# Optimization experiments

Hardware: AMD Instinct MI355X
Metric: run time of the kernel (lower is better)

The kernel has to match this reference:

```python
import jax, jax.numpy as jnp
import numpy as np

EPS = 1e-5
NUM_HEAD = 8
HEAD_DIM = 64
SCALE = HEAD_DIM ** -0.5


def setup_inputs() -> dict:
    key = jax.random.key(0)
    ks = jax.random.split(key, 3)
    b, n, dim = 4, 2048, 512
    inner = NUM_HEAD * HEAD_DIM  # 512
    x = jax.random.normal(ks[0], (b, n, dim), dtype=jnp.float32)
    ln_w = jnp.ones((dim,), jnp.float32)
    ln_b = jnp.zeros((dim,), jnp.float32)
    qkv_w = jax.random.normal(ks[1], (3 * inner, dim), jnp.float32) * (dim ** -0.5)
    qkv_b = jnp.zeros((3 * inner,), jnp.float32)
    out_w = jax.random.normal(ks[2], (dim, inner), jnp.float32) * (inner ** -0.5)
    out_b = jnp.zeros((dim,), jnp.float32)
    return {"x": x, "ln_w": ln_w, "ln_b": ln_b, "qkv_w": qkv_w,
            "qkv_b": qkv_b, "out_w": out_w, "out_b": out_b}


def reference(x, ln_w, ln_b, qkv_w, qkv_b, out_w, out_b):
    b, n, dim = x.shape
    # Pre-norm LayerNorm
    mu = jnp.mean(x, axis=-1, keepdims=True)
    var = jnp.mean(jnp.square(x - mu), axis=-1, keepdims=True)
    xn = (x - mu) * jax.lax.rsqrt(var + EPS) * ln_w + ln_b
    # QKV projection (torch Linear: y = x @ W.T + b)
    qkv = xn @ qkv_w.T + qkv_b  # [b, n, 3*inner]
    q, k, v = jnp.split(qkv, 3, axis=-1)
    def heads(t):  # [b, n, inner] -> [b, h, n, d]
        return t.reshape(b, n, NUM_HEAD, HEAD_DIM).transpose(0, 2, 1, 3)
    q, k, v = heads(q), heads(k), heads(v)
    # Naive full attention (materializes [b, h, n, n])
    dots = jnp.einsum('bhqd,bhkd->bhqk', q, k) * SCALE
    attn = jax.nn.softmax(dots, axis=-1)
    o = jnp.einsum('bhqk,bhkd->bhqd', attn, v)
    o = o.transpose(0, 2, 1, 3).reshape(b, n, NUM_HEAD * HEAD_DIM)
    return o @ out_w.T + out_b
```

## Files before the change

### kernel.cpp

```cpp
#include <hip/hip_runtime.h>

typedef __attribute__((ext_vector_type(8))) short bf16x8;
typedef __attribute__((ext_vector_type(4))) float floatx4;

#define B_    4
#define N_    2048
#define DIM_  512
#define NH_   8
#define HD_   64
#define SCALE_ 0.125f
#define SL2E_ (0.125f * 1.44269504f)

__device__ __forceinline__ unsigned short f32_to_bf16(float f) {
    return (unsigned short)((__float_as_uint(f) + 0x8000u) >> 16);
}

__device__ __forceinline__ float bf16_to_f32(unsigned short u) {
    return __uint_as_float(((unsigned int)u) << 16);
}

__device__ __forceinline__ floatx4 mfma16(bf16x8 a, bf16x8 b, floatx4 c) {
    return __builtin_amdgcn_mfma_f32_16x16x32_bf16(a, b, c, 0, 0, 0);
}

__device__ __forceinline__ floatx4 fzero4() {
    floatx4 z = {0.f, 0.f, 0.f, 0.f};
    return z;
}

__device__ __forceinline__ void async16(const unsigned short* g, unsigned short* l) {
    __builtin_amdgcn_global_load_lds((const __attribute__((address_space(1))) void*)g,
                                     (__attribute__((address_space(3))) void*)l,
                                     16, 0, 0);
}

__global__ __launch_bounds__(256) void ln_kernel(const float* __restrict__ x,
                                                 const float* __restrict__ w,
                                                 const float* __restrict__ b,
                                                 unsigned short* __restrict__ xn) {
    int wv = threadIdx.x >> 6;
    int lane = threadIdx.x & 63;
    int row = blockIdx.x * 4 + wv;
    const float4* xr = (const float4*)(x + (size_t)row * DIM_);
    float4 v0 = xr[lane * 2];
    float4 v1 = xr[lane * 2 + 1];
    float s  = (v0.x + v0.y + v0.z + v0.w) + (v1.x + v1.y + v1.z + v1.w);
    float sq = v0.x*v0.x + v0.y*v0.y + v0.z*v0.z + v0.w*v0.w +
               v1.x*v1.x + v1.y*v1.y + v1.z*v1.z + v1.w*v1.w;
#pragma unroll
    for (int off = 1; off < 64; off <<= 1) {
        s  += __shfl_xor(s, off, 64);
        sq += __shfl_xor(sq, off, 64);
    }
    float mu   = s * (1.f / DIM_);
    float var  = sq * (1.f / DIM_) - mu * mu;
    float rstd = rsqrtf(var + 1e-5f);
    float4 w0 = ((const float4*)w)[lane * 2];
    float4 w1 = ((const float4*)w)[lane * 2 + 1];
    float4 b0 = ((const float4*)b)[lane * 2];
    float4 b1 = ((const float4*)b)[lane * 2 + 1];
    float y[8];
    y[0] = (v0.x - mu) * rstd * w0.x + b0.x;
    y[1] = (v0.y - mu) * rstd * w0.y + b0.y;
    y[2] = (v0.z - mu) * rstd * w0.z + b0.z;
    y[3] = (v0.w - mu) * rstd * w0.w + b0.w;
    y[4] = (v1.x - mu) * rstd * w1.x + b1.x;
    y[5] = (v1.y - mu) * rstd * w1.y + b1.y;
    y[6] = (v1.z - mu) * rstd * w1.z + b1.z;
    y[7] = (v1.w - mu) * rstd * w1.w + b1.w;
    uint4 pk;
    pk.x = (unsigned int)f32_to_bf16(y[0]) | ((unsigned int)f32_to_bf16(y[1]) << 16);
    pk.y = (unsigned int)f32_to_bf16(y[2]) | ((unsigned int)f32_to_bf16(y[3]) << 16);
    pk.z = (unsigned int)f32_to_bf16(y[4]) | ((unsigned int)f32_to_bf16(y[5]) << 16);
    pk.w = (unsigned int)f32_to_bf16(y[6]) | ((unsigned int)f32_to_bf16(y[7]) << 16);
    ((uint4*)(xn + (size_t)row * DIM_))[lane] = pk;
}

__global__ __launch_bounds__(256) void cvt_kernel(const float* __restrict__ srcA, int na,
                                                  const float* __restrict__ srcB, int nb,
                                                  unsigned short* __restrict__ dstA,
                                                  unsigned short* __restrict__ dstB) {
    int idx = blockIdx.x * 256 + threadIdx.x;
    if (idx < na)            dstA[idx] = f32_to_bf16(srcA[idx]);
    else if (idx < na + nb)  dstB[idx - na] = f32_to_bf16(srcB[idx - na]);
}

#define GEMM_CORE512(A_, B_ptr, am0, bn0)                                           \
    __shared__ unsigned short Alds[2][128][32];                                     \
    __shared__ unsigned short Blds[2][128][32];                                     \
    int tid = threadIdx.x, lane = tid & 63, wid = tid >> 6;                         \
    int l15 = lane & 15, quad = lane >> 4;                                          \
    int wmloc = (wid >> 1) * 32, wnloc = (wid & 1) * 64;                            \
    int sr = lane >> 2;                                                             \
    int sc = (lane & 3) * 8;                                                        \
    int srow0 = 16 * wid;                                                           \
    floatx4 acc[2][4];                                                              \
    _Pragma("unroll")                                                               \
    for (int i = 0; i < 2; i++)                                                     \
        _Pragma("unroll")                                                           \
        for (int j = 0; j < 4; j++) acc[i][j] = fzero4();                           \
    int buf = 0;                                                                    \
    async16(A_ + (size_t)(am0 + srow0 + sr) * DIM_ + sc, &Alds[0][srow0][0]);       \
    async16(B_ptr + (size_t)(bn0 + srow0 + sr) * DIM_ + sc, &Blds[0][srow0][0]);    \
    __syncthreads();                                                                \
    for (int t = 0; t < 16; t++) {                                                  \
        if (t < 15) {                                                               \
            int k0 = (t + 1) * 32;                                                  \
            async16(A_ + (size_t)(am0 + srow0 + sr) * DIM_ + k0 + sc,               \
                    &Alds[buf ^ 1][srow0][0]);                                      \
            async16(B_ptr + (size_t)(bn0 + srow0 + sr) * DIM_ + k0 + sc,            \
                    &Blds[buf ^ 1][srow0][0]);                                      \
        }                                                                           \
        bf16x8 av[2], bv[4];                                                        \
        _Pragma("unroll")                                                           \
        for (int i = 0; i < 2; i++)                                                 \
            av[i] = *(const bf16x8*)(&Alds[buf][wmloc + 16 * i + l15][quad * 8]);   \
        _Pragma("unroll")                                                           \
        for (int j = 0; j < 4; j++)                                                 \
            bv[j] = *(const bf16x8*)(&Blds[buf][wnloc + 16 * j + l15][quad * 8]);   \
        _Pragma("unroll")                                                           \
        for (int i = 0; i < 2; i++)                                                 \
            _Pragma("unroll")                                                       \
            for (int j = 0; j < 4; j++)                                             \
                acc[i][j] = mfma16(av[i], bv[j], acc[i][j]);                        \
        __syncthreads();                                                            \
        buf ^= 1;                                                                   \
    }

__global__ __launch_bounds__(512, 4) void qkv_gemm(const unsigned short* __restrict__ A,
                                                   const unsigned short* __restrict__ Bw,
                                                   const float* __restrict__ bias,
                                                   unsigned short* __restrict__ Qh,
                                                   unsigned short* __restrict__ Kh,
                                                   unsigned short* __restrict__ Vt) {
    int am0 = blockIdx.x * 128, bn0 = blockIdx.y * 128;
    GEMM_CORE512(A, Bw, am0, bn0)

    if (bn0 >= 1024) {
        unsigned short* sc_ = &Alds[0][0][0] + wid * (16 * 40);
        int m0 = am0 + wmloc;
        int bidx = m0 >> 11;
        int t0 = m0 & 2047;
#pragma unroll
        for (int j = 0; j < 4; j++) {
            float bias_n = bias[bn0 + wnloc + 16 * j + l15];
#pragma unroll
            for (int i = 0; i < 2; i++)
#pragma unroll
                for (int r = 0; r < 4; r++)
                    sc_[l15 * 40 + 16 * i + quad * 4 + r] =
                        f32_to_bf16(acc[i][j][r] + bias_n);
            int nr = lane >> 2;
            int rem = (bn0 - 1024) + wnloc + 16 * j + nr;
            int head = rem >> 6, d = rem & 63;
            bf16x8 vv = *(const bf16x8*)(sc_ + nr * 40 + (lane & 3) * 8);
            *(bf16x8*)(Vt + ((size_t)(bidx * NH_ + head) * HD_ + d) * N_ +
                       t0 + (lane & 3) * 8) = vv;
        }
    } else {
#pragma unroll
        for (int i = 0; i < 2; i++) {
#pragma unroll
            for (int j = 0; j < 4; j++) {
                int n = bn0 + wnloc + 16 * j + l15;
                float bias_n = bias[n];
                int which = n >> 9;
                int rem = n & 511;
                int head = rem >> 6;
                int d = rem & 63;
#pragma unroll
                for (int r = 0; r < 4; r++) {
                    int m = am0 + wmloc + 16 * i + quad * 4 + r;
                    int b = m >> 11;
                    int t = m & 2047;
                    float val = acc[i][j][r] + bias_n;
                    if (which == 0) {
                        Qh[((size_t)(b * NH_ + head) * N_ + t) * HD_ + d] =
                            f32_to_bf16(val * SL2E_);
                    } else {
                        Kh[((size_t)(b * NH_ + head) * N_ + t) * HD_ + d] =
                            f32_to_bf16(val);
                    }
                }
            }
        }
    }
}

__global__ __launch_bounds__(256, 4) void out_gemm_fused(const unsigned short* __restrict__ Opart,
                                                         const float* __restrict__ lpart,
                                                         const unsigned short* __restrict__ Bw,
                                                         const float* __restrict__ bias,
                                                         float* __restrict__ out) {
    __shared__ unsigned short Alds[2][64][36];
    __shared__ unsigned short Blds[2][128][32];
    int tid = threadIdx.x, lane = tid & 63, wid = tid >> 6;
    int l15 = lane & 15, quad = lane >> 4;
    int wmloc = (wid >> 1) * 32, wnloc = (wid & 1) * 64;
    int am0 = blockIdx.x * 64, bn0 = blockIdx.y * 128;

    int arow = tid >> 2;
    int ac8 = (tid & 3) * 8;
    int token = am0 + arow;
    int bb = token >> 11;
    const size_t LSTR = (size_t)B_ * NH_ * N_;
    const size_t OSTR = (size_t)B_ * N_ * DIM_;
    const unsigned short* arow0 = Opart + (size_t)token * DIM_;
    const unsigned short* arow1 = arow0 + OSTR;

    int sr = lane >> 2;
    int sc = (lane & 3) * 8;

    floatx4 acc[2][4];
#pragma unroll
    for (int i = 0; i < 2; i++)
#pragma unroll
        for (int j = 0; j < 4; j++) acc[i][j] = fzero4();

#define STAGE_A(BUF, T)                                                         \
    {                                                                           \
        int k0 = (T) * 32;                                                      \
        int head = k0 >> 6;                                                     \
        size_t li = (size_t)(bb * NH_ + head) * N_ + (token & 2047);            \
        float l1 = lpart[li];                                                   \
        float l2 = lpart[LSTR + li];                                            \
        float inv = 1.f / (l1 + l2);                                            \
        float w1 = l1 * inv, w2 = l2 * inv;                                     \
        bf16x8 o0 = *(const bf16x8*)(arow0 + k0 + ac8);                         \
        bf16x8 o1 = *(const bf16x8*)(arow1 + k0 + ac8);                         \
        bf16x8 pk;                                                              \
        _Pragma("unroll")                                                       \
        for (int e = 0; e < 8; e++)                                             \
            pk[e] = (short)f32_to_bf16(                                         \
                w1 * bf16_to_f32((unsigned short)o0[e]) +                       \
                w2 * bf16_to_f32((unsigned short)o1[e]));                       \
        *(bf16x8*)(&Alds[BUF][arow][ac8]) = pk;                                 \
    }

#define STAGE_B(BUF, T)                                                         \
    {                                                                           \
        int k0 = (T) * 32;                                                      \
        _Pragma("unroll")                                                       \
        for (int i = 0; i < 2; i++) {                                           \
            int r0 = 32 * wid + 16 * i;                                         \
            async16(Bw + (size_t)(bn0 + r0 + sr) * DIM_ + k0 + sc,              \
                    &Blds[BUF][r0][0]);                                         \
        }                                                                       \
    }

    STAGE_B(0, 0)
    STAGE_A(0, 0)
    __syncthreads();
    int buf = 0;
    for (int t = 0; t < 16; t++) {
        if (t < 15) {
            STAGE_B(buf ^ 1, t + 1)
            STAGE_A(buf ^ 1, t + 1)
        }
        bf16x8 av[2], bv[4];
#pragma unroll
        for (int i = 0; i < 2; i++)
            av[i] = *(const bf16x8*)(&Alds[buf][wmloc + 16 * i + l15][quad * 8]);
#pragma unroll
        for (int j = 0; j < 4; j++)
            bv[j] = *(const bf16x8*)(&Blds[buf][wnloc + 16 * j + l15][quad * 8]);
#pragma unroll
        for (int i = 0; i < 2; i++)
#pragma unroll
            for (int j = 0; j < 4; j++)
                acc[i][j] = mfma16(av[i], bv[j], acc[i][j]);
        __syncthreads();
        buf ^= 1;
    }
#undef STAGE_A
#undef STAGE_B

#pragma unroll
    for (int i = 0; i < 2; i++) {
#pragma unroll
        for (int j = 0; j < 4; j++) {
            int n = bn0 + wnloc + 16 * j + l15;
            float bias_n = bias[n];
#pragma unroll
            for (int r = 0; r < 4; r++) {
                int m = am0 + wmloc + 16 * i + quad * 4 + r;
                out[(size_t)m * DIM_ + n] = acc[i][j][r] + bias_n;
            }
        }
    }
}

__global__ __launch_bounds__(256, 4) void attn_kernel(const unsigned short* __restrict__ Qh,
                                                      const unsigned short* __restrict__ Kh,
                                                      const unsigned short* __restrict__ Vtg,
                                                      unsigned short* __restrict__ Opart,
                                                      float* __restrict__ lpart) {
    int bh = blockIdx.y;
    int b = bh >> 3, head = bh & 7;
    int qt = blockIdx.x;
    int split = blockIdx.z;
    int kv0 = split << 10;
    int tid = threadIdx.x, lane = tid & 63, w = tid >> 6;
    int l15 = lane & 15, quad = lane >> 4;

    const unsigned short* Qp = Qh + (size_t)bh * N_ * HD_;
    const unsigned short* Kg = Kh + (size_t)bh * N_ * HD_;
    const unsigned short* Vg = Vtg + (size_t)bh * HD_ * N_;

    int q0 = qt * 128 + w * 32;

    bf16x8 aQ[2][2];
#pragma unroll
    for (int mh = 0; mh < 2; mh++) {
        const unsigned short* qrow = Qp + (size_t)(q0 + mh * 16 + l15) * HD_ + quad * 8;
        aQ[mh][0] = *(const bf16x8*)(qrow);
        aQ[mh][1] = *(const bf16x8*)(qrow + 32);
    }

    floatx4 of[2][4];
#pragma unroll
    for (int mh = 0; mh < 2; mh++)
#pragma unroll
        for (int t = 0; t < 4; t++) of[mh][t] = fzero4();
    floatx4 lacc[2];
    lacc[0] = fzero4(); lacc[1] = fzero4();

    const short onebf = (short)0x3F80;
    bf16x8 ones = {onebf, onebf, onebf, onebf, onebf, onebf, onebf, onebf};

    __shared__ unsigned short Kt[64][64];
    __shared__ unsigned short Vs[64][64];
    __shared__ unsigned short Pl[4][32][72];

    int srow = lane >> 3;
    int scol = ((lane & 7) ^ srow) * 8;

    int swz0 = (quad ^ (l15 & 7)) * 8;
    int swz1 = ((quad + 4) ^ (l15 & 7)) * 8;

    unsigned short* myP = &Pl[w][0][0];
    for (int kv = kv0; kv < kv0 + 1024; kv += 64) {
#pragma unroll
        for (int i = 0; i < 2; i++) {
            int r0 = 16 * w + 8 * i;
            async16(Kg + (size_t)(kv + r0 + srow) * HD_ + scol, &Kt[r0][0]);
            async16(Vg + (size_t)(r0 + srow) * N_ + kv + scol, &Vs[r0][0]);
        }
        __syncthreads();
        bf16x8 kf[8];
#pragma unroll
        for (int h = 0; h < 4; h++) {
            kf[2 * h]     = *(const bf16x8*)(&Kt[16 * h + l15][swz0]);
            kf[2 * h + 1] = *(const bf16x8*)(&Kt[16 * h + l15][swz1]);
        }
#pragma unroll
        for (int mh = 0; mh < 2; mh++) {
            floatx4 c[4];
#pragma unroll
            for (int h = 0; h < 4; h++) {
                floatx4 cc = fzero4();
                cc = mfma16(aQ[mh][0], kf[2 * h], cc);
                cc = mfma16(aQ[mh][1], kf[2 * h + 1], cc);
                c[h] = cc;
            }
            unsigned short* pw = myP + (mh * 16 + quad * 4) * 72 + l15;
#pragma unroll
            for (int h = 0; h < 4; h++)
#pragma unroll
                for (int r = 0; r < 4; r++)
                    pw[r * 72 + h * 16] = f32_to_bf16(exp2f(c[h][r]));
        }
        bf16x8 vf[8];
#pragma unroll
        for (int t = 0; t < 4; t++) {
            vf[2 * t]     = *(const bf16x8*)(&Vs[16 * t + l15][swz0]);
            vf[2 * t + 1] = *(const bf16x8*)(&Vs[16 * t + l15][swz1]);
        }
#pragma unroll
        for (int mh = 0; mh < 2; mh++) {
            const unsigned short* pr = myP + (mh * 16 + l15) * 72;
            bf16x8 aP0 = *(const bf16x8*)(pr + quad * 8);
            bf16x8 aP1 = *(const bf16x8*)(pr + 32 + quad * 8);
#pragma unroll
            for (int t = 0; t < 4; t++) {
                of[mh][t] = mfma16(aP0, vf[2 * t], of[mh][t]);
                of[mh][t] = mfma16(aP1, vf[2 * t + 1], of[mh][t]);
            }
            lacc[mh] = mfma16(aP0, ones, lacc[mh]);
            lacc[mh] = mfma16(aP1, ones, lacc[mh]);
        }
        __syncthreads();
    }

    unsigned short* Od = Opart + (size_t)split * B_ * N_ * DIM_;
#pragma unroll
    for (int mh = 0; mh < 2; mh++) {
        float inv[4];
#pragma unroll
        for (int r = 0; r < 4; r++) inv[r] = 1.f / lacc[mh][r];
#pragma unroll
        for (int t = 0; t < 4; t++) {
#pragma unroll
            for (int r = 0; r < 4; r++) {
                int t_tok = q0 + mh * 16 + quad * 4 + r;
                int d = 16 * t + l15;
                Od[((size_t)b * N_ + t_tok) * DIM_ + head * HD_ + d] =
                    f32_to_bf16(of[mh][t][r] * inv[r]);
            }
        }
        if (l15 == 0) {
#pragma unroll
            for (int r = 0; r < 4; r++) {
                int t_tok = q0 + mh * 16 + quad * 4 + r;
                lpart[(size_t)split * B_ * NH_ * N_ + (size_t)bh * N_ + t_tok] =
                    lacc[mh][r];
            }
        }
    }
}

extern "C" void kernel_launch(void* const* d_in, const int* in_sizes, int n_in,
                              void* d_out, int out_size, void* d_ws, size_t ws_size,
                              hipStream_t stream) {
    const float* x     = (const float*)d_in[0];
    const float* ln_w  = (const float*)d_in[1];
    const float* ln_b  = (const float*)d_in[2];
    const float* qkv_w = (const float*)d_in[3];
    const float* qkv_b = (const float*)d_in[4];
    const float* out_w = (const float*)d_in[5];
    const float* out_b = (const float*)d_in[6];
    float* out = (float*)d_out;

    char* ws = (char*)d_ws;
    const size_t TOK = (size_t)B_ * N_;
    unsigned short* xn    = (unsigned short*)ws;  ws += TOK * DIM_ * 2;
    unsigned short* wq_bf = (unsigned short*)ws;  ws += (size_t)3 * DIM_ * DIM_ * 2;
    unsigned short* wo_bf = (unsigned short*)ws;  ws += (size_t)DIM_ * DIM_ * 2;
    unsigned short* Qh    = (unsigned short*)ws;  ws += TOK * DIM_ * 2;
    unsigned short* Kh    = (unsigned short*)ws;  ws += TOK * DIM_ * 2;
    unsigned short* Vt    = (unsigned short*)ws;  ws += TOK * DIM_ * 2;
    unsigned short* Opart = (unsigned short*)ws;  ws += (size_t)2 * TOK * DIM_ * 2;
    float*          lpart = (float*)ws;           ws += (size_t)2 * B_ * NH_ * N_ * 4;

    const int NW = 3 * DIM_ * DIM_;
    const int NO = DIM_ * DIM_;

    ln_kernel<<<TOK / 4, 256, 0, stream>>>(x, ln_w, ln_b, xn);
    cvt_kernel<<<(NW + NO + 255) / 256, 256, 0, stream>>>(qkv_w, NW, out_w, NO, wq_bf, wo_bf);
    qkv_gemm<<<dim3(TOK / 128, (3 * DIM_) / 128), 512, 0, stream>>>(xn, wq_bf, qkv_b, Qh, Kh, Vt);
    attn_kernel<<<dim3(N_ / 128, B_ * NH_, 2), 256, 0, stream>>>(Qh, Kh, Vt, Opart, lpart);
    out_gemm_fused<<<dim3(TOK / 64, DIM_ / 128), 256, 0, stream>>>(Opart, lpart, wo_bf, out_b, out);
}
```

Baseline: 175.5 us.

## Rewrite attention inner loop with 32x32 MFMA, register-resident P, double-buffered KV

Replaces the 16x16x32 MFMA attention loop with 32x32x16 MFMAs that compute S^T so the exponentiated probabilities stay in registers. They are packed with cvt_pk_bf16 and permlane32_swap, which removes the per-wave LDS round trip for P. The row-sum is accumulated in VALU instead of extra MFMAs against a ones vector. K/V tiles are double-buffered so the next tile's async load overlaps compute, and s_setprio hints are added around the MFMA blocks. The cost is higher register pressure from the floatx16 accumulators and double the LDS for K/V, which may reduce occupancy under the launch bounds of 256 threads and 4 blocks.

```diff
diff --git a/kernel.cpp b/kernel.cpp
--- a/kernel.cpp
+++ b/kernel.cpp
@@ -2,6 +2,8 @@
 
 typedef __attribute__((ext_vector_type(8))) short bf16x8;
 typedef __attribute__((ext_vector_type(4))) float floatx4;
+typedef __attribute__((ext_vector_type(16))) float floatx16;
+typedef __attribute__((ext_vector_type(4))) unsigned int uintx4;
 
 #define B_    4
 #define N_    2048
@@ -23,9 +25,26 @@
     return __builtin_amdgcn_mfma_f32_16x16x32_bf16(a, b, c, 0, 0, 0);
 }
 
+__device__ __forceinline__ floatx16 mfma32(bf16x8 a, bf16x8 b, floatx16 c) {
+    return __builtin_amdgcn_mfma_f32_32x32x16_bf16(a, b, c, 0, 0, 0);
+}
+
 __device__ __forceinline__ floatx4 fzero4() {
     floatx4 z = {0.f, 0.f, 0.f, 0.f};
     return z;
+}
+
+__device__ __forceinline__ floatx16 fzero16() {
+    floatx16 z;
+#pragma unroll
+    for (int i = 0; i < 16; i++) z[i] = 0.f;
+    return z;
+}
+
+__device__ __forceinline__ unsigned int cvt_pk_bf16(float lo, float hi) {
+    unsigned int r;
+    asm("v_cvt_pk_bf16_f32 %0, %1, %2" : "=v"(r) : "v"(lo), "v"(hi));
+    return r;
 }
 
 __device__ __forceinline__ void async16(const unsigned short* g, unsigned short* l) {
@@ -301,7 +320,8 @@
     int split = blockIdx.z;
     int kv0 = split << 10;
     int tid = threadIdx.x, lane = tid & 63, w = tid >> 6;
-    int l15 = lane & 15, quad = lane >> 4;
+    int l31 = lane & 31, hi = lane >> 5;
+    int xr = l31 & 7;
 
     const unsigned short* Qp = Qh + (size_t)bh * N_ * HD_;
     const unsigned short* Kg = Kh + (size_t)bh * N_ * HD_;
@@ -309,113 +329,115 @@
 
     int q0 = qt * 128 + w * 32;
 
-    bf16x8 aQ[2][2];
-#pragma unroll
-    for (int mh = 0; mh < 2; mh++) {
-        const unsigned short* qrow = Qp + (size_t)(q0 + mh * 16 + l15) * HD_ + quad * 8;
-        aQ[mh][0] = *(const bf16x8*)(qrow);
-        aQ[mh][1] = *(const bf16x8*)(qrow + 32);
-    }
-
-    floatx4 of[2][4];
-#pragma unroll
-    for (int mh = 0; mh < 2; mh++)
-#pragma unroll
-        for (int t = 0; t < 4; t++) of[mh][t] = fzero4();
-    floatx4 lacc[2];
-    lacc[0] = fzero4(); lacc[1] = fzero4();
-
-    const short onebf = (short)0x3F80;
-    bf16x8 ones = {onebf, onebf, onebf, onebf, onebf, onebf, onebf, onebf};
-
-    __shared__ unsigned short Kt[64][64];
-    __shared__ unsigned short Vs[64][64];
-    __shared__ unsigned short Pl[4][32][72];
+    bf16x8 aQ[4];
+    {
+        const unsigned short* qrow = Qp + (size_t)(q0 + l31) * HD_ + hi * 8;
+#pragma unroll
+        for (int t = 0; t < 4; t++)
+            aQ[t] = *(const bf16x8*)(qrow + 16 * t);
+    }
+
+    __shared__ unsigned short Kt[2][64][64];
+    __shared__ unsigned short Vs[2][64][64];
+    __shared__ float l_sm[4][32];
 
     int srow = lane >> 3;
     int scol = ((lane & 7) ^ srow) * 8;
 
-    int swz0 = (quad ^ (l15 & 7)) * 8;
-    int swz1 = ((quad + 4) ^ (l15 & 7)) * 8;
-
-    unsigned short* myP = &Pl[w][0][0];
-    for (int kv = kv0; kv < kv0 + 1024; kv += 64) {
-#pragma unroll
-        for (int i = 0; i < 2; i++) {
-            int r0 = 16 * w + 8 * i;
-            async16(Kg + (size_t)(kv + r0 + srow) * HD_ + scol, &Kt[r0][0]);
-            async16(Vg + (size_t)(r0 + srow) * N_ + kv + scol, &Vs[r0][0]);
-        }
+#define STAGE_KV(BUF, KV)                                                           \
+    {                                                                               \
+        _Pragma("unroll")                                                           \
+        for (int i = 0; i < 2; i++) {                                               \
+            int r0 = 16 * w + 8 * i;                                                \
+            async16(Kg + (size_t)((KV) + r0 + srow) * HD_ + scol, &Kt[BUF][r0][0]); \
+            async16(Vg + (size_t)(r0 + srow) * N_ + (KV) + scol, &Vs[BUF][r0][0]);  \
+        }                                                                           \
+    }
+
+    STAGE_KV(0, kv0)
+    __syncthreads();
+
+    floatx16 of[2];
+    of[0] = fzero16();
+    of[1] = fzero16();
+    float lsumA = 0.f, lsumB = 0.f;
+
+    int buf = 0;
+    for (int it = 0; it < 16; it++) {
+        if (it < 15) {
+            STAGE_KV(buf ^ 1, kv0 + (it + 1) * 64)
+        }
+        bf16x8 pa[4];
+#pragma unroll
+        for (int tau = 0; tau < 2; tau++) {
+            bf16x8 kf[4];
+#pragma unroll
+            for (int t = 0; t < 4; t++)
+                kf[t] = *(const bf16x8*)(&Kt[buf][32 * tau + l31][((2 * t + hi) ^ xr) * 8]);
+            floatx16 acc = fzero16();
+            __builtin_amdgcn_s_setprio(1);
+#pragma unroll
+            for (int t = 0; t < 4; t++)
+                acc = mfma32(kf[t], aQ[t], acc);
+            __builtin_amdgcn_s_setprio(0);
+            float p[16];
+#pragma unroll
+            for (int r = 0; r < 16; r += 2) {
+                p[r]     = exp2f(acc[r]);
+                p[r + 1] = exp2f(acc[r + 1]);
+                lsumA += p[r];
+                lsumB += p[r + 1];
+            }
+            unsigned int a0 = cvt_pk_bf16(p[0], p[1]);
+            unsigned int b0 = cvt_pk_bf16(p[4], p[5]);
+            unsigned int a1 = cvt_pk_bf16(p[2], p[3]);
+            unsigned int b1 = cvt_pk_bf16(p[6], p[7]);
+            unsigned int a2 = cvt_pk_bf16(p[8], p[9]);
+            unsigned int b2 = cvt_pk_bf16(p[12], p[13]);
+            unsigned int a3 = cvt_pk_bf16(p[10], p[11]);
+            unsigned int b3 = cvt_pk_bf16(p[14], p[15]);
+            asm("v_permlane32_swap_b32 %0, %1" : "+v"(a0), "+v"(b0));
+            asm("v_permlane32_swap_b32 %0, %1" : "+v"(a1), "+v"(b1));
+            asm("v_permlane32_swap_b32 %0, %1" : "+v"(a2), "+v"(b2));
+            asm("v_permlane32_swap_b32 %0, %1" : "+v"(a3), "+v"(b3));
+            uintx4 f0 = {a0, a1, b0, b1};
+            uintx4 f1 = {a2, a3, b2, b3};
+            pa[2 * tau]     = __builtin_bit_cast(bf16x8, f0);
+            pa[2 * tau + 1] = __builtin_bit_cast(bf16x8, f1);
+        }
+        __builtin_amdgcn_s_setprio(1);
+#pragma unroll
+        for (int s = 0; s < 4; s++) {
+#pragma unroll
+            for (int dt = 0; dt < 2; dt++) {
+                bf16x8 vf = *(const bf16x8*)(&Vs[buf][32 * dt + l31][((2 * s + hi) ^ xr) * 8]);
+                of[dt] = mfma32(pa[s], vf, of[dt]);
+            }
+        }
+        __builtin_amdgcn_s_setprio(0);
         __syncthreads();
-        bf16x8 kf[8];
-#pragma unroll
-        for (int h = 0; h < 4; h++) {
-            kf[2 * h]     = *(const bf16x8*)(&Kt[16 * h + l15][swz0]);
-            kf[2 * h + 1] = *(const bf16x8*)(&Kt[16 * h + l15][swz1]);
-        }
-#pragma unroll
-        for (int mh = 0; mh < 2; mh++) {
-            floatx4 c[4];
-#pragma unroll
-            for (int h = 0; h < 4; h++) {
-                floatx4 cc = fzero4();
-                cc = mfma16(aQ[mh][0], kf[2 * h], cc);
-                cc = mfma16(aQ[mh][1], kf[2 * h + 1], cc);
-                c[h] = cc;
-            }
-            unsigned short* pw = myP + (mh * 16 + quad * 4) * 72 + l15;
-#pragma unroll
-            for (int h = 0; h < 4; h++)
-#pragma unroll
-                for (int r = 0; r < 4; r++)
-                    pw[r * 72 + h * 16] = f32_to_bf16(exp2f(c[h][r]));
-        }
-        bf16x8 vf[8];
-#pragma unroll
-        for (int t = 0; t < 4; t++) {
-            vf[2 * t]     = *(const bf16x8*)(&Vs[16 * t + l15][swz0]);
-            vf[2 * t + 1] = *(const bf16x8*)(&Vs[16 * t + l15][swz1]);
-        }
-#pragma unroll
-        for (int mh = 0; mh < 2; mh++) {
-            const unsigned short* pr = myP + (mh * 16 + l15) * 72;
-            bf16x8 aP0 = *(const bf16x8*)(pr + quad * 8);
-            bf16x8 aP1 = *(const bf16x8*)(pr + 32 + quad * 8);
-#pragma unroll
-            for (int t = 0; t < 4; t++) {
-                of[mh][t] = mfma16(aP0, vf[2 * t], of[mh][t]);
-                of[mh][t] = mfma16(aP1, vf[2 * t + 1], of[mh][t]);
-            }
-            lacc[mh] = mfma16(aP0, ones, lacc[mh]);
-            lacc[mh] = mfma16(aP1, ones, lacc[mh]);
-        }
-        __syncthreads();
-    }
+        buf ^= 1;
+    }
+#undef STAGE_KV
+
+    float lsum = lsumA + lsumB;
+    lsum += __shfl_xor(lsum, 32, 64);
+    if (lane < 32) {
+        l_sm[w][l31] = 1.f / lsum;
+        lpart[(size_t)split * B_ * NH_ * N_ + (size_t)bh * N_ + q0 + l31] = lsum;
+    }
+    __syncthreads();
 
     unsigned short* Od = Opart + (size_t)split * B_ * N_ * DIM_;
 #pragma unroll
-    for (int mh = 0; mh < 2; mh++) {
-        float inv[4];
-#pragma unroll
-        for (int r = 0; r < 4; r++) inv[r] = 1.f / lacc[mh][r];
-#pragma unroll
-        for (int t = 0; t < 4; t++) {
-#pragma unroll
-            for (int r = 0; r < 4; r++) {
-                int t_tok = q0 + mh * 16 + quad * 4 + r;
-                int d = 16 * t + l15;
-                Od[((size_t)b * N_ + t_tok) * DIM_ + head * HD_ + d] =
-                    f32_to_bf16(of[mh][t][r] * inv[r]);
-            }
-        }
-        if (l15 == 0) {
-#pragma unroll
-            for (int r = 0; r < 4; r++) {
-                int t_tok = q0 + mh * 16 + quad * 4 + r;
-                lpart[(size_t)split * B_ * NH_ * N_ + (size_t)bh * N_ + t_tok] =
-                    lacc[mh][r];
-            }
-        }
+    for (int r = 0; r < 16; r++) {
+        int qr = (r & 3) + 8 * (r >> 2) + 4 * hi;
+        float inv = l_sm[w][qr];
+        int token = q0 + qr;
+        size_t base = ((size_t)b * N_ + token) * DIM_ + (size_t)head * HD_;
+#pragma unroll
+        for (int dt = 0; dt < 2; dt++)
+            Od[base + 32 * dt + l31] = f32_to_bf16(of[dt][r] * inv);
     }
 }
 
```

Result: slower. 181.0 us (+3.1%).
